# Kernel tuning notes

Hardware: AMD Instinct MI355X
Metric: run time of the kernel (lower is better)

The kernel has to match this reference:

```python
import jax, jax.numpy as jnp
import numpy as np

DIM = 512
HEADS = 8
DIM_HEAD = 64
INNER = HEADS * DIM_HEAD
SCALE = DIM_HEAD ** -0.5


def setup_inputs() -> dict:
    key = jax.random.key(0)
    k1, k2, k3, k4 = jax.random.split(key, 4)
    x = jax.random.normal(k1, (2, 4096, DIM), dtype=jnp.float32)
    # torch Linear stores weight [out, in]; we keep [in, out] for x @ W
    W_qkv = jax.random.normal(k2, (DIM, 3 * INNER), dtype=jnp.float32) * (DIM ** -0.5)
    W_out = jax.random.normal(k3, (INNER, DIM), dtype=jnp.float32) * (INNER ** -0.5)
    b_out = jax.random.normal(k4, (DIM,), dtype=jnp.float32) * 0.01
    return {"x": x, "W_qkv": W_qkv, "W_out": W_out, "b_out": b_out}


def reference(x, W_qkv, W_out, b_out):
    b, l, _ = x.shape
    qkv = x @ W_qkv  # [b, l, 3*inner]
    q, k, v = jnp.split(qkv, 3, axis=-1)

    def split_heads(t):  # [b, l, inner] -> [b, h, l, d]
        return t.reshape(b, l, HEADS, DIM_HEAD).transpose(0, 2, 1, 3)

    q, k, v = split_heads(q), split_heads(k), split_heads(v)
    attn = jnp.einsum('bhid,bhjd->bhij', q, k) * SCALE
    attn = jax.nn.softmax(attn, axis=-1)
    attned = jnp.einsum('bhij,bhjd->bhid', attn, v)
    attned = attned.transpose(0, 2, 1, 3).reshape(b, l, INNER)
    return attned @ W_out + b_out
```

## Files before the change

kernel.cpp:

```cpp
#include <hip/hip_runtime.h>

typedef short bf16x8 __attribute__((ext_vector_type(8)));
typedef float f32x4 __attribute__((ext_vector_type(4)));

#define MFMA16(a, b, c) __builtin_amdgcn_mfma_f32_16x16x32_bf16((a), (b), (c), 0, 0, 0)

__device__ __forceinline__ unsigned short f2bf(float f) {
    union { float f; unsigned u; } v; v.f = f;
    unsigned r = v.u + 0x7FFFu + ((v.u >> 16) & 1u);
    return (unsigned short)(r >> 16);
}
__device__ __forceinline__ float bf2f(unsigned short s) {
    union { unsigned u; float f; } v; v.u = (unsigned)s << 16;
    return v.f;
}

__global__ __launch_bounds__(256) void k_cvt(const float* __restrict__ in,
                                             unsigned short* __restrict__ out, int n4) {
    int i = blockIdx.x * 256 + threadIdx.x;
    if (i < n4) {
        float4 v = reinterpret_cast<const float4*>(in)[i];
        ushort4 o;
        o.x = f2bf(v.x); o.y = f2bf(v.y); o.z = f2bf(v.z); o.w = f2bf(v.w);
        reinterpret_cast<ushort4*>(out)[i] = o;
    }
}

__global__ __launch_bounds__(256) void k_tr(const float* __restrict__ in,
                                            unsigned short* __restrict__ out, int R, int C) {
    __shared__ float t[64][65];
    int c0 = blockIdx.x * 64, r0 = blockIdx.y * 64;
    int lc = threadIdx.x & 63, lr4 = threadIdx.x >> 6;
#pragma unroll
    for (int j = 0; j < 16; ++j) {
        int r = lr4 + j * 4;
        t[r][lc] = in[(size_t)(r0 + r) * C + c0 + lc];
    }
    __syncthreads();
#pragma unroll
    for (int j = 0; j < 16; ++j) {
        int c = lr4 + j * 4;
        out[(size_t)(c0 + c) * R + r0 + lc] = f2bf(t[lc][c]);
    }
}

__device__ __forceinline__ void gemm_main_512(const unsigned short* __restrict__ A,
                                              const unsigned short* __restrict__ Bt,
                                              int m0, int n0,
                                              unsigned short* AL, unsigned short* BL,
                                              f32x4 acc[4][4]) {
    const int tid = threadIdx.x;
    const int lane = tid & 63, wid = tid >> 6;
    const int wr = wid >> 1, wc = wid & 1;
    const int lg = lane >> 4, lr = lane & 15;

    for (int k0 = 0; k0 < 512; k0 += 32) {
#pragma unroll
        for (int i = 0; i < 2; ++i) {
            int idx = tid + i * 256;
            int row = idx >> 2;
            int c8 = (idx & 3) * 8;
            *reinterpret_cast<bf16x8*>(&AL[row * 40 + c8]) =
                *reinterpret_cast<const bf16x8*>(&A[(size_t)(m0 + row) * 512 + k0 + c8]);
            *reinterpret_cast<bf16x8*>(&BL[row * 40 + c8]) =
                *reinterpret_cast<const bf16x8*>(&Bt[(size_t)(n0 + row) * 512 + k0 + c8]);
        }
        __syncthreads();
        bf16x8 af[4], bfr[4];
#pragma unroll
        for (int rt = 0; rt < 4; ++rt)
            af[rt] = *reinterpret_cast<const bf16x8*>(&AL[(wr * 64 + rt * 16 + lr) * 40 + lg * 8]);
#pragma unroll
        for (int ct = 0; ct < 4; ++ct)
            bfr[ct] = *reinterpret_cast<const bf16x8*>(&BL[(wc * 64 + ct * 16 + lr) * 40 + lg * 8]);
#pragma unroll
        for (int rt = 0; rt < 4; ++rt)
#pragma unroll
            for (int ct = 0; ct < 4; ++ct)
                acc[rt][ct] = MFMA16(af[rt], bfr[ct], acc[rt][ct]);
        __syncthreads();
    }
}

__global__ __launch_bounds__(256) void k_gemm_qkv(const unsigned short* __restrict__ X,
                                                  const unsigned short* __restrict__ Wt,
                                                  unsigned short* __restrict__ Qb,
                                                  unsigned short* __restrict__ Kb,
                                                  unsigned short* __restrict__ VbT) {
    __shared__ __align__(16) unsigned short AL[128 * 40];
    __shared__ __align__(16) unsigned short BL[128 * 40];
    f32x4 acc[4][4];
#pragma unroll
    for (int i = 0; i < 4; ++i)
#pragma unroll
        for (int j = 0; j < 4; ++j) acc[i][j] = (f32x4){0.f, 0.f, 0.f, 0.f};

    int m0 = blockIdx.x * 128, n0 = blockIdx.y * 128;
    gemm_main_512(X, Wt, m0, n0, AL, BL, acc);

    const int tid = threadIdx.x;
    const int lane = tid & 63, wid = tid >> 6;
    const int wr = wid >> 1, wc = wid & 1;
    const int lg = lane >> 4, lr = lane & 15;
    const int which = n0 >> 9;
#pragma unroll
    for (int rt = 0; rt < 4; ++rt) {
#pragma unroll
        for (int ct = 0; ct < 4; ++ct) {
            int col = n0 + wc * 64 + ct * 16 + lr;
            int inner = col & 511;
            int h = inner >> 6, d = inner & 63;
            int row0 = m0 + wr * 64 + rt * 16 + lg * 4;
            int b = row0 >> 12, l0 = row0 & 4095;
            if (which == 0) {
#pragma unroll
                for (int j = 0; j < 4; ++j)
                    Qb[(((size_t)(b * 8 + h)) * 4096 + l0 + j) * 64 + d] =
                        f2bf(acc[rt][ct][j] * 0.18033688f);
            } else if (which == 1) {
#pragma unroll
                for (int j = 0; j < 4; ++j)
                    Kb[(((size_t)(b * 8 + h)) * 4096 + l0 + j) * 64 + d] = f2bf(acc[rt][ct][j]);
            } else {
                ushort4 o;
                o.x = f2bf(acc[rt][ct][0]); o.y = f2bf(acc[rt][ct][1]);
                o.z = f2bf(acc[rt][ct][2]); o.w = f2bf(acc[rt][ct][3]);
                *reinterpret_cast<ushort4*>(
                    &VbT[(((size_t)(b * 8 + h)) * 64 + d) * 4096 + l0]) = o;
            }
        }
    }
}

__global__ __launch_bounds__(256) void k_gemm_out(const unsigned short* __restrict__ An,
                                                  const unsigned short* __restrict__ Wot,
                                                  const float* __restrict__ bout,
                                                  float* __restrict__ out) {
    __shared__ __align__(16) unsigned short AL[128 * 40];
    __shared__ __align__(16) unsigned short BL[128 * 40];
    f32x4 acc[4][4];
#pragma unroll
    for (int i = 0; i < 4; ++i)
#pragma unroll
        for (int j = 0; j < 4; ++j) acc[i][j] = (f32x4){0.f, 0.f, 0.f, 0.f};

    int m0 = blockIdx.x * 128, n0 = blockIdx.y * 128;
    gemm_main_512(An, Wot, m0, n0, AL, BL, acc);

    const int tid = threadIdx.x;
    const int lane = tid & 63, wid = tid >> 6;
    const int wr = wid >> 1, wc = wid & 1;
    const int lg = lane >> 4, lr = lane & 15;
#pragma unroll
    for (int rt = 0; rt < 4; ++rt) {
#pragma unroll
        for (int ct = 0; ct < 4; ++ct) {
            int col = n0 + wc * 64 + ct * 16 + lr;
            float bv = bout[col];
#pragma unroll
            for (int j = 0; j < 4; ++j) {
                int row = m0 + wr * 64 + rt * 16 + lg * 4 + j;
                out[(size_t)row * 512 + col] = acc[rt][ct][j] + bv;
            }
        }
    }
}

__global__ __launch_bounds__(256) void k_attn(const unsigned short* __restrict__ Q,
                                              const unsigned short* __restrict__ K,
                                              const unsigned short* __restrict__ VT,
                                              unsigned short* __restrict__ Op0,
                                              unsigned short* __restrict__ Op1,
                                              float* __restrict__ Lp) {
    __shared__ __align__(16) unsigned short KL[64 * 72];
    __shared__ __align__(16) unsigned short VTl[64 * 72];
    __shared__ __align__(16) unsigned short PL[4][32 * 72];

    const int qt = blockIdx.x;
    const int bh = blockIdx.y;
    const int hh = blockIdx.z;
    const size_t base = (size_t)bh * 4096 * 64;
    const int kvbase = hh * 2048;
    const int tid = threadIdx.x, lane = tid & 63, wid = tid >> 6;
    const int lg = lane >> 4, lr = lane & 15;
    const int q0 = qt * 128 + wid * 32;

    bf16x8 qf[2][2];
#pragma unroll
    for (int rt = 0; rt < 2; ++rt)
#pragma unroll
        for (int kt = 0; kt < 2; ++kt)
            qf[rt][kt] = *reinterpret_cast<const bf16x8*>(
                &Q[base + (size_t)(q0 + rt * 16 + lr) * 64 + kt * 32 + lg * 8]);

    f32x4 oacc[2][4];
    f32x4 sacc[2];
#pragma unroll
    for (int rt = 0; rt < 2; ++rt) {
        sacc[rt] = (f32x4){0.f, 0.f, 0.f, 0.f};
#pragma unroll
        for (int dt = 0; dt < 4; ++dt) oacc[rt][dt] = (f32x4){0.f, 0.f, 0.f, 0.f};
    }

    bf16x8 ones;
#pragma unroll
    for (int j = 0; j < 8; ++j) ones[j] = (short)0x3F80;

    const int r0 = tid >> 3, c0 = (tid & 7) * 8;

    bf16x8 kreg[2], vreg[2];
#pragma unroll
    for (int i = 0; i < 2; ++i) {
        kreg[i] = *reinterpret_cast<const bf16x8*>(
            &K[base + (size_t)(kvbase + r0 + i * 32) * 64 + c0]);
        vreg[i] = *reinterpret_cast<const bf16x8*>(
            &VT[base + (size_t)(r0 + i * 32) * 4096 + kvbase + c0]);
    }
#pragma unroll
    for (int i = 0; i < 2; ++i) {
        *reinterpret_cast<bf16x8*>(&KL[(r0 + i * 32) * 72 + c0]) = kreg[i];
        *reinterpret_cast<bf16x8*>(&VTl[(r0 + i * 32) * 72 + c0]) = vreg[i];
    }
    __syncthreads();

    for (int kv = 0; kv < 32; ++kv) {
        const int kv0n = kvbase + kv * 64 + 64;
        if (kv < 31) {
#pragma unroll
            for (int i = 0; i < 2; ++i) {
                kreg[i] = *reinterpret_cast<const bf16x8*>(
                    &K[base + (size_t)(kv0n + r0 + i * 32) * 64 + c0]);
                vreg[i] = *reinterpret_cast<const bf16x8*>(
                    &VT[base + (size_t)(r0 + i * 32) * 4096 + kv0n + c0]);
            }
        }

        f32x4 s[2][4];
#pragma unroll
        for (int rt = 0; rt < 2; ++rt)
#pragma unroll
            for (int ct = 0; ct < 4; ++ct) s[rt][ct] = (f32x4){0.f, 0.f, 0.f, 0.f};
        __builtin_amdgcn_s_setprio(1);
#pragma unroll
        for (int kt = 0; kt < 2; ++kt) {
#pragma unroll
            for (int ct = 0; ct < 4; ++ct) {
                bf16x8 kf = *reinterpret_cast<const bf16x8*>(
                    &KL[(ct * 16 + lr) * 72 + kt * 32 + lg * 8]);
#pragma unroll
                for (int rt = 0; rt < 2; ++rt)
                    s[rt][ct] = MFMA16(qf[rt][kt], kf, s[rt][ct]);
            }
        }
        __builtin_amdgcn_s_setprio(0);

#pragma unroll
        for (int rt = 0; rt < 2; ++rt)
#pragma unroll
            for (int ct = 0; ct < 4; ++ct)
#pragma unroll
                for (int j = 0; j < 4; ++j)
                    PL[wid][(rt * 16 + lg * 4 + j) * 72 + ct * 16 + lr] =
                        f2bf(__builtin_amdgcn_exp2f(s[rt][ct][j]));

        __builtin_amdgcn_s_setprio(1);
#pragma unroll
        for (int kt = 0; kt < 2; ++kt) {
            bf16x8 pf[2];
#pragma unroll
            for (int rt = 0; rt < 2; ++rt)
                pf[rt] = *reinterpret_cast<const bf16x8*>(
                    &PL[wid][(rt * 16 + lr) * 72 + kt * 32 + lg * 8]);
#pragma unroll
            for (int dt = 0; dt < 4; ++dt) {
                bf16x8 vf = *reinterpret_cast<const bf16x8*>(
                    &VTl[(dt * 16 + lr) * 72 + kt * 32 + lg * 8]);
#pragma unroll
                for (int rt = 0; rt < 2; ++rt)
                    oacc[rt][dt] = MFMA16(pf[rt], vf, oacc[rt][dt]);
            }
#pragma unroll
            for (int rt = 0; rt < 2; ++rt)
                sacc[rt] = MFMA16(pf[rt], ones, sacc[rt]);
        }
        __builtin_amdgcn_s_setprio(0);

        __syncthreads();
        if (kv < 31) {
#pragma unroll
            for (int i = 0; i < 2; ++i) {
                *reinterpret_cast<bf16x8*>(&KL[(r0 + i * 32) * 72 + c0]) = kreg[i];
                *reinterpret_cast<bf16x8*>(&VTl[(r0 + i * 32) * 72 + c0]) = vreg[i];
            }
        }
        __syncthreads();
    }

    unsigned short* Op = hh ? Op1 : Op0;
    const int b = bh >> 3, h = bh & 7;
#pragma unroll
    for (int rt = 0; rt < 2; ++rt) {
#pragma unroll
        for (int j = 0; j < 4; ++j) {
            int row = q0 + rt * 16 + lg * 4 + j;
#pragma unroll
            for (int dt = 0; dt < 4; ++dt) {
                int d = dt * 16 + lr;
                Op[((size_t)b * 4096 + row) * 512 + h * 64 + d] = f2bf(oacc[rt][dt][j]);
            }
            if (lr == 0)
                Lp[((size_t)(hh * 16 + bh)) * 4096 + row] = sacc[rt][j];
        }
    }
}

__global__ __launch_bounds__(256) void k_reduce(const unsigned short* __restrict__ O0,
                                                const unsigned short* __restrict__ O1,
                                                const float* __restrict__ Lp,
                                                unsigned short* __restrict__ An) {
    int i4 = blockIdx.x * 256 + threadIdx.x;
    int e = i4 * 4;
    int r = e >> 9;
    int c = e & 511, h = c >> 6;
    int b = r >> 12, l = r & 4095;
    int lidx = (b * 8 + h) * 4096 + l;
    float inv = 1.f / (Lp[lidx] + Lp[16 * 4096 + lidx]);
    ushort4 a = *reinterpret_cast<const ushort4*>(&O0[e]);
    ushort4 bq = *reinterpret_cast<const ushort4*>(&O1[e]);
    ushort4 o;
    o.x = f2bf((bf2f(a.x) + bf2f(bq.x)) * inv);
    o.y = f2bf((bf2f(a.y) + bf2f(bq.y)) * inv);
    o.z = f2bf((bf2f(a.z) + bf2f(bq.z)) * inv);
    o.w = f2bf((bf2f(a.w) + bf2f(bq.w)) * inv);
    *reinterpret_cast<ushort4*>(&An[e]) = o;
}

extern "C" void kernel_launch(void* const* d_in, const int* in_sizes, int n_in,
                              void* d_out, int out_size, void* d_ws, size_t ws_size,
                              hipStream_t stream) {
    const float* x    = (const float*)d_in[0];
    const float* Wqkv = (const float*)d_in[1];
    const float* Wout = (const float*)d_in[2];
    const float* bout = (const float*)d_in[3];
    float* out = (float*)d_out;

    char* ws = (char*)d_ws;
    unsigned short* Xbf  = (unsigned short*)(ws);
    unsigned short* Wqkt = (unsigned short*)(ws + 8388608);
    unsigned short* Wot  = (unsigned short*)(ws + 8388608 + 1572864);
    unsigned short* Qb   = (unsigned short*)(ws + 10485760);
    unsigned short* Kb   = (unsigned short*)(ws + 18874368);
    unsigned short* VbT  = (unsigned short*)(ws + 27262976);
    unsigned short* An   = (unsigned short*)(ws + 35651584);
    unsigned short* Op0  = Xbf;
    unsigned short* Op1  = An;
    float*          Lp   = (float*)(ws + 8388608);

    k_cvt<<<4096, 256, 0, stream>>>(x, Xbf, 4194304 / 4);
    k_tr<<<dim3(24, 8), 256, 0, stream>>>(Wqkv, Wqkt, 512, 1536);
    k_tr<<<dim3(8, 8), 256, 0, stream>>>(Wout, Wot, 512, 512);
    k_gemm_qkv<<<dim3(64, 12), 256, 0, stream>>>(Xbf, Wqkt, Qb, Kb, VbT);
    k_attn<<<dim3(32, 16, 2), 256, 0, stream>>>(Qb, Kb, VbT, Op0, Op1, Lp);
    k_reduce<<<4096, 256, 0, stream>>>(Op0, Op1, Lp, An);
    k_gemm_out<<<dim3(64, 4), 256, 0, stream>>>(An, Wot, bout, out);
}
```

Baseline: 239.1 us.

## Load K/V fragments directly from global memory, drop LDS staging and barriers

The attention kernel stops staging K and V^T tiles through shared memory. Each wave now loads its MFMA K fragments straight into registers (prefetching the next tile) and reads V^T fragments from global memory, which removes the two block-wide barriers per iteration. The grid is also flattened so that consecutive blocks cover different (batch, head, half) pairs. The cost is that all four waves fetch the same K/V data redundantly through L1/L2, and V loads sit on the critical path with no prefetch.

```diff
diff --git a/kernel.cpp b/kernel.cpp
--- a/kernel.cpp
+++ b/kernel.cpp
@@ -172,13 +172,12 @@
                                               unsigned short* __restrict__ Op0,
                                               unsigned short* __restrict__ Op1,
                                               float* __restrict__ Lp) {
-    __shared__ __align__(16) unsigned short KL[64 * 72];
-    __shared__ __align__(16) unsigned short VTl[64 * 72];
     __shared__ __align__(16) unsigned short PL[4][32 * 72];
 
-    const int qt = blockIdx.x;
-    const int bh = blockIdx.y;
-    const int hh = blockIdx.z;
+    const int flat = blockIdx.x;
+    const int bhh  = flat & 31;
+    const int qt   = flat >> 5;
+    const int bh = bhh >> 1, hh = bhh & 1;
     const size_t base = (size_t)bh * 4096 * 64;
     const int kvbase = hh * 2048;
     const int tid = threadIdx.x, lane = tid & 63, wid = tid >> 6;
@@ -206,34 +205,16 @@
 #pragma unroll
     for (int j = 0; j < 8; ++j) ones[j] = (short)0x3F80;
 
-    const int r0 = tid >> 3, c0 = (tid & 7) * 8;
-
-    bf16x8 kreg[2], vreg[2];
-#pragma unroll
-    for (int i = 0; i < 2; ++i) {
-        kreg[i] = *reinterpret_cast<const bf16x8*>(
-            &K[base + (size_t)(kvbase + r0 + i * 32) * 64 + c0]);
-        vreg[i] = *reinterpret_cast<const bf16x8*>(
-            &VT[base + (size_t)(r0 + i * 32) * 4096 + kvbase + c0]);
-    }
-#pragma unroll
-    for (int i = 0; i < 2; ++i) {
-        *reinterpret_cast<bf16x8*>(&KL[(r0 + i * 32) * 72 + c0]) = kreg[i];
-        *reinterpret_cast<bf16x8*>(&VTl[(r0 + i * 32) * 72 + c0]) = vreg[i];
-    }
-    __syncthreads();
+    bf16x8 kfr[2][4];
+#pragma unroll
+    for (int kt = 0; kt < 2; ++kt)
+#pragma unroll
+        for (int ct = 0; ct < 4; ++ct)
+            kfr[kt][ct] = *reinterpret_cast<const bf16x8*>(
+                &K[base + (size_t)(kvbase + ct * 16 + lr) * 64 + kt * 32 + lg * 8]);
 
     for (int kv = 0; kv < 32; ++kv) {
-        const int kv0n = kvbase + kv * 64 + 64;
-        if (kv < 31) {
-#pragma unroll
-            for (int i = 0; i < 2; ++i) {
-                kreg[i] = *reinterpret_cast<const bf16x8*>(
-                    &K[base + (size_t)(kv0n + r0 + i * 32) * 64 + c0]);
-                vreg[i] = *reinterpret_cast<const bf16x8*>(
-                    &VT[base + (size_t)(r0 + i * 32) * 4096 + kv0n + c0]);
-            }
-        }
+        const int kv0 = kvbase + kv * 64;
 
         f32x4 s[2][4];
 #pragma unroll
@@ -242,17 +223,23 @@
             for (int ct = 0; ct < 4; ++ct) s[rt][ct] = (f32x4){0.f, 0.f, 0.f, 0.f};
         __builtin_amdgcn_s_setprio(1);
 #pragma unroll
-        for (int kt = 0; kt < 2; ++kt) {
-#pragma unroll
-            for (int ct = 0; ct < 4; ++ct) {
-                bf16x8 kf = *reinterpret_cast<const bf16x8*>(
-                    &KL[(ct * 16 + lr) * 72 + kt * 32 + lg * 8]);
+        for (int kt = 0; kt < 2; ++kt)
+#pragma unroll
+            for (int ct = 0; ct < 4; ++ct)
 #pragma unroll
                 for (int rt = 0; rt < 2; ++rt)
-                    s[rt][ct] = MFMA16(qf[rt][kt], kf, s[rt][ct]);
-            }
-        }
+                    s[rt][ct] = MFMA16(qf[rt][kt], kfr[kt][ct], s[rt][ct]);
         __builtin_amdgcn_s_setprio(0);
+
+        if (kv < 31) {
+            const int kv0n = kv0 + 64;
+#pragma unroll
+            for (int kt = 0; kt < 2; ++kt)
+#pragma unroll
+                for (int ct = 0; ct < 4; ++ct)
+                    kfr[kt][ct] = *reinterpret_cast<const bf16x8*>(
+                        &K[base + (size_t)(kv0n + ct * 16 + lr) * 64 + kt * 32 + lg * 8]);
+        }
 
 #pragma unroll
         for (int rt = 0; rt < 2; ++rt)
@@ -274,7 +261,7 @@
 #pragma unroll
             for (int dt = 0; dt < 4; ++dt) {
                 bf16x8 vf = *reinterpret_cast<const bf16x8*>(
-                    &VTl[(dt * 16 + lr) * 72 + kt * 32 + lg * 8]);
+                    &VT[base + (size_t)(dt * 16 + lr) * 4096 + kv0 + kt * 32 + lg * 8]);
 #pragma unroll
                 for (int rt = 0; rt < 2; ++rt)
                     oacc[rt][dt] = MFMA16(pf[rt], vf, oacc[rt][dt]);
@@ -284,16 +271,6 @@
                 sacc[rt] = MFMA16(pf[rt], ones, sacc[rt]);
         }
         __builtin_amdgcn_s_setprio(0);
-
-        __syncthreads();
-        if (kv < 31) {
-#pragma unroll
-            for (int i = 0; i < 2; ++i) {
-                *reinterpret_cast<bf16x8*>(&KL[(r0 + i * 32) * 72 + c0]) = kreg[i];
-                *reinterpret_cast<bf16x8*>(&VTl[(r0 + i * 32) * 72 + c0]) = vreg[i];
-            }
-        }
-        __syncthreads();
     }
 
     unsigned short* Op = hh ? Op1 : Op0;
@@ -360,7 +337,7 @@
     k_tr<<<dim3(24, 8), 256, 0, stream>>>(Wqkv, Wqkt, 512, 1536);
     k_tr<<<dim3(8, 8), 256, 0, stream>>>(Wout, Wot, 512, 512);
     k_gemm_qkv<<<dim3(64, 12), 256, 0, stream>>>(Xbf, Wqkt, Qb, Kb, VbT);
-    k_attn<<<dim3(32, 16, 2), 256, 0, stream>>>(Qb, Kb, VbT, Op0, Op1, Lp);
+    k_attn<<<dim3(1024), 256, 0, stream>>>(Qb, Kb, VbT, Op0, Op1, Lp);
     k_reduce<<<4096, 256, 0, stream>>>(Op0, Op1, Lp, An);
     k_gemm_out<<<dim3(64, 4), 256, 0, stream>>>(An, Wot, bout, out);
 }
```

Result: slower. 374.0 us (+56.5%).
